# Performance work log

Measured on AMD Instinct MI355X. Metric: run time of the kernel, lower is better.

Reference implementation:

```python
import jax, jax.numpy as jnp
import numpy as np

MODEL_DIM = 1024
NUM_HEADS = 16
HEAD_DIM = MODEL_DIM // NUM_HEADS
WINDOW = 4


def local_mask(seq_len):
    i = jnp.arange(seq_len)
    return jnp.abs(i[:, None] - i[None, :]) <= WINDOW  # [S,S] bool


def setup_inputs() -> dict:
    key = jax.random.key(0)
    ks = jax.random.split(key, 9)
    d = MODEL_DIM
    s = 0.02
    return {
        "x": jax.random.normal(ks[0], (4, 2048, d), dtype=jnp.float32),
        "Wq": jax.random.normal(ks[1], (d, d), dtype=jnp.float32) * s,
        "bq": jnp.zeros((d,), dtype=jnp.float32),
        "Wk": jax.random.normal(ks[2], (d, d), dtype=jnp.float32) * s,
        "bk": jnp.zeros((d,), dtype=jnp.float32),
        "Wv": jax.random.normal(ks[3], (d, d), dtype=jnp.float32) * s,
        "bv": jnp.zeros((d,), dtype=jnp.float32),
        "Wo": jax.random.normal(ks[4], (d, d), dtype=jnp.float32) * s,
        "bo": jnp.zeros((d,), dtype=jnp.float32),
    }


def reference(x, Wq, bq, Wk, bk, Wv, bv, Wo, bo):
    B, S, D = x.shape
    H, Hd = NUM_HEADS, HEAD_DIM
    # linear projections (torch Linear: x @ W.T + b; here W stored pre-transposed)
    q = (x @ Wq + bq).reshape(B, S, H, Hd).transpose(0, 2, 1, 3)  # [B,H,S,Hd]
    k = (x @ Wk + bk).reshape(B, S, H, Hd).transpose(0, 2, 1, 3)
    v = (x @ Wv + bv).reshape(B, S, H, Hd).transpose(0, 2, 1, 3)
    scores = jnp.einsum("bhqd,bhkd->bhqk", q, k) / jnp.sqrt(jnp.float32(Hd))
    mask = local_mask(S)[None, None]  # [1,1,S,S]
    scores = jnp.where(mask, scores, -jnp.inf)
    weights = jax.nn.softmax(scores, axis=-1)  # [B,H,S,S]
    out = jnp.einsum("bhqk,bhkd->bhqd", weights, v)
    out = out.transpose(0, 2, 1, 3).reshape(B, S, D)
    out = out @ Wo + bo
    return (out, weights)
```

## Files before the change

### kernel.cpp

```cpp
#include <hip/hip_runtime.h>


typedef __attribute__((ext_vector_type(8))) short short8;
typedef __attribute__((ext_vector_type(4))) float f32x4;

#define B_    4
#define S_    2048
#define D_    1024
#define H_    16
#define HD_   64
#define WIN_  4
#define NROW  (B_ * S_)
#define OUT0_ELEMS  ((size_t)B_ * S_ * D_)
#define TOTAL_CH  67108864ull
#define ZQKV_CH   18874368ull

__device__ __forceinline__ unsigned short f2bf(float f) {
  unsigned int u = __float_as_uint(f);
  u += 0x7fffu + ((u >> 16) & 1u);
  return (unsigned short)(u >> 16);
}
__device__ __forceinline__ float bf2f(unsigned short u) {
  return __uint_as_float(((unsigned int)u) << 16);
}

__device__ __forceinline__ void zstore(f32x4* __restrict__ woutv, size_t g) {
  int row = (int)(g >> 9);
  int f = (int)(g & 511);
  int s = row & (S_ - 1);
  int f0 = (s > WIN_) ? ((s - WIN_) >> 2) : 0;
  int hi = (s + WIN_ < S_ - 1) ? (s + WIN_) : (S_ - 1);
  int f1 = hi >> 2;
  if (f < f0 || f > f1) {
    f32x4 z = {0.f, 0.f, 0.f, 0.f};
    __builtin_nontemporal_store(z, woutv + g);
  }
}

__global__ __launch_bounds__(256) void xconv_k(const float* __restrict__ x,
                                               unsigned short* __restrict__ o) {
  int i = blockIdx.x * 256 + threadIdx.x;
  float4 f = reinterpret_cast<const float4*>(x)[i];
  ushort4 u;
  u.x = f2bf(f.x); u.y = f2bf(f.y); u.z = f2bf(f.z); u.w = f2bf(f.w);
  reinterpret_cast<ushort4*>(o)[i] = u;
}

__global__ __launch_bounds__(256) void wconv_k(const float* __restrict__ W0,
                                               const float* __restrict__ W1,
                                               const float* __restrict__ W2,
                                               const float* __restrict__ W3,
                                               unsigned short* __restrict__ out) {
  __shared__ float t[32][33];
  const float* Ws[4] = {W0, W1, W2, W3};
  const float* W = Ws[blockIdx.z];
  unsigned short* o = out + (size_t)blockIdx.z * D_ * D_;
  int tx = threadIdx.x;
  int ty = threadIdx.y;
  int n0 = blockIdx.x * 32, k0 = blockIdx.y * 32;
#pragma unroll
  for (int i = 0; i < 4; ++i)
    t[ty + 8 * i][tx] = W[(size_t)(k0 + ty + 8 * i) * D_ + (n0 + tx)];
  __syncthreads();
#pragma unroll
  for (int i = 0; i < 4; ++i)
    o[(size_t)(n0 + ty + 8 * i) * D_ + (k0 + tx)] = f2bf(t[tx][ty + 8 * i]);
}

#define GLD16(g, l)                                                            \
  __builtin_amdgcn_global_load_lds(                                            \
      (const __attribute__((address_space(1))) unsigned int*)(g),              \
      (__attribute__((address_space(3))) unsigned int*)(l), 16, 0, 0)

__global__ __launch_bounds__(256) void gemm_qkv_k(
    const unsigned short* __restrict__ A, const unsigned short* __restrict__ Wt,
    const float* __restrict__ bq, const float* __restrict__ bk,
    const float* __restrict__ bv, unsigned short* __restrict__ Qb,
    unsigned short* __restrict__ Kb, unsigned short* __restrict__ Vb,
    float* __restrict__ wout) {
  __shared__ unsigned short As[128 * 64];
  __shared__ unsigned short Bs[128 * 64];
  const int g = blockIdx.x;
  const int o = g & 7, gg = g >> 3;
  const int row0 = (o * 8 + (gg & 7)) * 128;
  const int col0 = (gg >> 3) * 128;

  const int tid = threadIdx.x;
  const int lane = tid & 63;
  const int wid = tid >> 6;
  const int wm = wid >> 1, wn = wid & 1;
  f32x4* woutv = (f32x4*)wout;

  f32x4 acc[4][4] = {};
  const int frow = lane & 15;
  const int cpb = lane >> 4;

  for (int kt = 0; kt < 16; ++kt) {
#pragma unroll
    for (int j = 0; j < 3; ++j)
      zstore(woutv, (size_t)(kt * 3 + j) * 393216u + (unsigned)g * 256u + tid);
#pragma unroll
    for (int i = 0; i < 4; ++i) {
      int c = tid + (i << 8);
      int r = c >> 3;
      int jj = (c & 7) ^ (r & 7);
      GLD16(A + (size_t)(row0 + r) * D_ + (kt << 6) + (jj << 3),
            (char*)As + c * 16);
      GLD16(Wt + (size_t)(col0 + r) * D_ + (kt << 6) + (jj << 3),
            (char*)Bs + c * 16);
    }
    __syncthreads();
#pragma unroll
    for (int ks = 0; ks < 2; ++ks) {
      short8 af[4], bfr[4];
#pragma unroll
      for (int mi = 0; mi < 4; ++mi) {
        int row = wm * 64 + mi * 16 + frow;
        int swz = (ks * 4 + cpb) ^ (row & 7);
        af[mi] = *reinterpret_cast<const short8*>((char*)As + row * 128 + swz * 16);
      }
#pragma unroll
      for (int ni = 0; ni < 4; ++ni) {
        int row = wn * 64 + ni * 16 + frow;
        int swz = (ks * 4 + cpb) ^ (row & 7);
        bfr[ni] = *reinterpret_cast<const short8*>((char*)Bs + row * 128 + swz * 16);
      }
#pragma unroll
      for (int mi = 0; mi < 4; ++mi)
#pragma unroll
        for (int ni = 0; ni < 4; ++ni)
          acc[mi][ni] = __builtin_amdgcn_mfma_f32_16x16x32_bf16(
              af[mi], bfr[ni], acc[mi][ni], 0, 0, 0);
    }
    __syncthreads();
  }

#pragma unroll
  for (int mi = 0; mi < 4; ++mi) {
#pragma unroll
    for (int ni = 0; ni < 4; ++ni) {
#pragma unroll
      for (int r = 0; r < 4; ++r) {
        int gr = row0 + wm * 64 + mi * 16 + ((lane >> 4) << 2) + r;
        int gc = col0 + wn * 64 + ni * 16 + (lane & 15);
        int z = gc >> 10;
        int ci = gc & 1023;
        float bias = (z == 0) ? bq[ci] : (z == 1) ? bk[ci] : bv[ci];
        unsigned short* outp = (z == 0) ? Qb : (z == 1) ? Kb : Vb;
        int bb = gr >> 11, s = gr & (S_ - 1);
        int h = ci >> 6, hd = ci & 63;
        outp[(((size_t)(bb * H_ + h) * S_ + s) << 6) + hd] =
            f2bf(acc[mi][ni][r] + bias);
      }
    }
  }
}

__global__ __launch_bounds__(256) void gemm_out_k(
    const unsigned short* __restrict__ A, const unsigned short* __restrict__ Bt,
    const float* __restrict__ bias, float* __restrict__ o_) {
  __shared__ unsigned short As[128 * 64];
  __shared__ unsigned short Bs[128 * 64];
  const int g = blockIdx.x;
  const int o = g & 7, gg = g >> 3;
  const int row0 = (o * 8 + (gg & 7)) * 128;
  const int col0 = (gg >> 3) * 128;

  const int tid = threadIdx.x;
  const int lane = tid & 63;
  const int wid = tid >> 6;
  const int wm = wid >> 1, wn = wid & 1;

  f32x4 acc[4][4] = {};
  const int frow = lane & 15;
  const int cpb = lane >> 4;

  for (int kt = 0; kt < 16; ++kt) {
#pragma unroll
    for (int i = 0; i < 4; ++i) {
      int c = tid + (i << 8);
      int r = c >> 3;
      int jj = (c & 7) ^ (r & 7);
      GLD16(A + (size_t)(row0 + r) * D_ + (kt << 6) + (jj << 3),
            (char*)As + c * 16);
      GLD16(Bt + (size_t)(col0 + r) * D_ + (kt << 6) + (jj << 3),
            (char*)Bs + c * 16);
    }
    __syncthreads();
#pragma unroll
    for (int ks = 0; ks < 2; ++ks) {
      short8 af[4], bfr[4];
#pragma unroll
      for (int mi = 0; mi < 4; ++mi) {
        int row = wm * 64 + mi * 16 + frow;
        int swz = (ks * 4 + cpb) ^ (row & 7);
        af[mi] = *reinterpret_cast<const short8*>((char*)As + row * 128 + swz * 16);
      }
#pragma unroll
      for (int ni = 0; ni < 4; ++ni) {
        int row = wn * 64 + ni * 16 + frow;
        int swz = (ks * 4 + cpb) ^ (row & 7);
        bfr[ni] = *reinterpret_cast<const short8*>((char*)Bs + row * 128 + swz * 16);
      }
#pragma unroll
      for (int mi = 0; mi < 4; ++mi)
#pragma unroll
        for (int ni = 0; ni < 4; ++ni)
          acc[mi][ni] = __builtin_amdgcn_mfma_f32_16x16x32_bf16(
              af[mi], bfr[ni], acc[mi][ni], 0, 0, 0);
    }
    __syncthreads();
  }

#pragma unroll
  for (int mi = 0; mi < 4; ++mi) {
#pragma unroll
    for (int ni = 0; ni < 4; ++ni) {
#pragma unroll
      for (int r = 0; r < 4; ++r) {
        int gr = row0 + wm * 64 + mi * 16 + ((lane >> 4) << 2) + r;
        int gc = col0 + wn * 64 + ni * 16 + (lane & 15);
        o_[(size_t)gr * D_ + gc] = acc[mi][ni][r] + bias[gc];
      }
    }
  }
}

__global__ __launch_bounds__(256) void attn_k(const unsigned short* __restrict__ Q,
                                              const unsigned short* __restrict__ K,
                                              const unsigned short* __restrict__ V,
                                              float* __restrict__ wout,
                                              unsigned short* __restrict__ attn) {
  int lane = threadIdx.x & 63;
  int wid = threadIdx.x >> 6;
  int row = blockIdx.x * 4 + wid;
  int s = row & (S_ - 1);
  int bh = row >> 11;
  int b = bh >> 4, h = bh & 15;
  float qd = bf2f(Q[(size_t)row * HD_ + lane]);
  const unsigned short* Kb = K + (size_t)bh * S_ * HD_;
  const unsigned short* Vb = V + (size_t)bh * S_ * HD_;

  float sc[9];
#pragma unroll
  for (int j = 0; j < 9; ++j) {
    int ks = s - WIN_ + j;
    bool ok = (ks >= 0) && (ks < S_);
    float v = ok ? qd * bf2f(Kb[(size_t)ks * HD_ + lane]) : 0.f;
#pragma unroll
    for (int off = 32; off > 0; off >>= 1) v += __shfl_xor(v, off, 64);
    sc[j] = ok ? v * 0.125f : -INFINITY;
  }
  float m = sc[0];
#pragma unroll
  for (int j = 1; j < 9; ++j) m = fmaxf(m, sc[j]);
  float w[9];
  float sum = 0.f;
#pragma unroll
  for (int j = 0; j < 9; ++j) { w[j] = __expf(sc[j] - m); sum += w[j]; }
  float inv = 1.f / sum;
#pragma unroll
  for (int j = 0; j < 9; ++j) w[j] *= inv;

  float o = 0.f;
#pragma unroll
  for (int j = 0; j < 9; ++j) {
    int ks = s - WIN_ + j;
    if (ks >= 0 && ks < S_) o += w[j] * bf2f(Vb[(size_t)ks * HD_ + lane]);
  }
  attn[((size_t)(b * S_ + s)) * D_ + h * HD_ + lane] = f2bf(o);

  const int lo = s - WIN_;
  const int hiq = (s + WIN_ < S_ - 1) ? (s + WIN_) : (S_ - 1);
  const int f0 = (s > WIN_) ? ((s - WIN_) >> 2) : 0;
  const int f1 = hiq >> 2;
  f32x4* rowp = reinterpret_cast<f32x4*>(wout + (size_t)row * S_);
  if (lane <= f1 - f0) {
    f32x4 v4;
#pragma unroll
    for (int e = 0; e < 4; ++e) {
      int d = ((f0 + lane) << 2) + e - lo;
      float val = 0.f;
#pragma unroll
      for (int j = 0; j < 9; ++j)
        if (d == j) val = w[j];
      v4[e] = val;
    }
    __builtin_nontemporal_store(v4, rowp + f0 + lane);
  }

  unsigned int gtid = blockIdx.x * 256u + threadIdx.x;
#pragma unroll
  for (int k2 = 0; k2 < 6; ++k2) {
    size_t g = ZQKV_CH + (size_t)k2 * 8388608u + gtid;
    if (g < TOTAL_CH) zstore((f32x4*)wout, g);
  }
}

extern "C" void kernel_launch(void* const* d_in, const int* in_sizes, int n_in,
                              void* d_out, int out_size, void* d_ws,
                              size_t ws_size, hipStream_t stream) {
  const float* x = (const float*)d_in[0];
  const float* Wq = (const float*)d_in[1];
  const float* bq = (const float*)d_in[2];
  const float* Wk = (const float*)d_in[3];
  const float* bk = (const float*)d_in[4];
  const float* Wv = (const float*)d_in[5];
  const float* bv = (const float*)d_in[6];
  const float* Wo = (const float*)d_in[7];
  const float* bo = (const float*)d_in[8];
  float* out = (float*)d_out;
  float* wout = out + OUT0_ELEMS;

  char* ws = (char*)d_ws;
  unsigned short* x_bf = (unsigned short*)(ws);
  unsigned short* Wt = (unsigned short*)(ws + (16ull << 20));
  unsigned short* Qb = (unsigned short*)(ws + (24ull << 20));
  unsigned short* Kb = (unsigned short*)(ws + (40ull << 20));
  unsigned short* Vb = (unsigned short*)(ws + (56ull << 20));
  unsigned short* attn = (unsigned short*)(ws + (72ull << 20));

  xconv_k<<<NROW * D_ / 1024, 256, 0, stream>>>(x, x_bf);
  wconv_k<<<dim3(32, 32, 4), dim3(32, 8), 0, stream>>>(Wq, Wk, Wv, Wo, Wt);
  gemm_qkv_k<<<1536, 256, 0, stream>>>(x_bf, Wt, bq, bk, bv, Qb, Kb, Vb, wout);
  attn_k<<<(B_ * H_ * S_) / 4, 256, 0, stream>>>(Qb, Kb, Vb, wout, attn);
  gemm_out_k<<<512, 256, 0, stream>>>(attn, Wt + (size_t)3 * D_ * D_, bo, out);
}
```

Measured before the change: 285.6 us.

## Move all weight-matrix zero stores into attention kernel with full-row writes

Stops spreading zero-fill of the huge dense attention-weights output across the QKV GEMM and the attention kernel. Instead, each attention wave now writes its entire 2048-wide row, zeros plus the nine softmax weights, with coalesced nontemporal vector stores. This removes per-chunk index arithmetic and frees the GEMM from interleaved global stores. The trade-off is that the write bandwidth no longer overlaps GEMM compute, and the attention kernel becomes purely store-bound.

```diff
diff --git a/kernel.cpp b/kernel.cpp
--- a/kernel.cpp
+++ b/kernel.cpp
@@ -12,8 +12,6 @@
 #define WIN_  4
 #define NROW  (B_ * S_)
 #define OUT0_ELEMS  ((size_t)B_ * S_ * D_)
-#define TOTAL_CH  67108864ull
-#define ZQKV_CH   18874368ull
 
 __device__ __forceinline__ unsigned short f2bf(float f) {
   unsigned int u = __float_as_uint(f);
@@ -22,19 +20,6 @@
 }
 __device__ __forceinline__ float bf2f(unsigned short u) {
   return __uint_as_float(((unsigned int)u) << 16);
-}
-
-__device__ __forceinline__ void zstore(f32x4* __restrict__ woutv, size_t g) {
-  int row = (int)(g >> 9);
-  int f = (int)(g & 511);
-  int s = row & (S_ - 1);
-  int f0 = (s > WIN_) ? ((s - WIN_) >> 2) : 0;
-  int hi = (s + WIN_ < S_ - 1) ? (s + WIN_) : (S_ - 1);
-  int f1 = hi >> 2;
-  if (f < f0 || f > f1) {
-    f32x4 z = {0.f, 0.f, 0.f, 0.f};
-    __builtin_nontemporal_store(z, woutv + g);
-  }
 }
 
 __global__ __launch_bounds__(256) void xconv_k(const float* __restrict__ x,
@@ -76,8 +61,7 @@
     const unsigned short* __restrict__ A, const unsigned short* __restrict__ Wt,
     const float* __restrict__ bq, const float* __restrict__ bk,
     const float* __restrict__ bv, unsigned short* __restrict__ Qb,
-    unsigned short* __restrict__ Kb, unsigned short* __restrict__ Vb,
-    float* __restrict__ wout) {
+    unsigned short* __restrict__ Kb, unsigned short* __restrict__ Vb) {
   __shared__ unsigned short As[128 * 64];
   __shared__ unsigned short Bs[128 * 64];
   const int g = blockIdx.x;
@@ -89,16 +73,12 @@
   const int lane = tid & 63;
   const int wid = tid >> 6;
   const int wm = wid >> 1, wn = wid & 1;
-  f32x4* woutv = (f32x4*)wout;
 
   f32x4 acc[4][4] = {};
   const int frow = lane & 15;
   const int cpb = lane >> 4;
 
   for (int kt = 0; kt < 16; ++kt) {
-#pragma unroll
-    for (int j = 0; j < 3; ++j)
-      zstore(woutv, (size_t)(kt * 3 + j) * 393216u + (unsigned)g * 256u + tid);
 #pragma unroll
     for (int i = 0; i < 4; ++i) {
       int c = tid + (i << 8);
@@ -270,30 +250,26 @@
   }
   attn[((size_t)(b * S_ + s)) * D_ + h * HD_ + lane] = f2bf(o);
 
+  f32x4* rowp = reinterpret_cast<f32x4*>(wout + (size_t)row * S_);
   const int lo = s - WIN_;
-  const int hiq = (s + WIN_ < S_ - 1) ? (s + WIN_) : (S_ - 1);
-  const int f0 = (s > WIN_) ? ((s - WIN_) >> 2) : 0;
-  const int f1 = hiq >> 2;
-  f32x4* rowp = reinterpret_cast<f32x4*>(wout + (size_t)row * S_);
-  if (lane <= f1 - f0) {
-    f32x4 v4;
-#pragma unroll
-    for (int e = 0; e < 4; ++e) {
-      int d = ((f0 + lane) << 2) + e - lo;
-      float val = 0.f;
-#pragma unroll
-      for (int j = 0; j < 9; ++j)
-        if (d == j) val = w[j];
-      v4[e] = val;
-    }
-    __builtin_nontemporal_store(v4, rowp + f0 + lane);
-  }
-
-  unsigned int gtid = blockIdx.x * 256u + threadIdx.x;
-#pragma unroll
-  for (int k2 = 0; k2 < 6; ++k2) {
-    size_t g = ZQKV_CH + (size_t)k2 * 8388608u + gtid;
-    if (g < TOTAL_CH) zstore((f32x4*)wout, g);
+  const int hi = s + WIN_;
+#pragma unroll
+  for (int i = 0; i < 8; ++i) {
+    int f = lane + (i << 6);
+    int c0 = f << 2;
+    f32x4 v4 = {0.f, 0.f, 0.f, 0.f};
+    if (c0 + 3 >= lo && c0 <= hi) {
+#pragma unroll
+      for (int e = 0; e < 4; ++e) {
+        int d = c0 + e - lo;
+        float val = 0.f;
+#pragma unroll
+        for (int j = 0; j < 9; ++j)
+          if (d == j) val = w[j];
+        v4[e] = val;
+      }
+    }
+    __builtin_nontemporal_store(v4, rowp + f);
   }
 }
 
@@ -322,7 +298,7 @@
 
   xconv_k<<<NROW * D_ / 1024, 256, 0, stream>>>(x, x_bf);
   wconv_k<<<dim3(32, 32, 4), dim3(32, 8), 0, stream>>>(Wq, Wk, Wv, Wo, Wt);
-  gemm_qkv_k<<<1536, 256, 0, stream>>>(x_bf, Wt, bq, bk, bv, Qb, Kb, Vb, wout);
+  gemm_qkv_k<<<1536, 256, 0, stream>>>(x_bf, Wt, bq, bk, bv, Qb, Kb, Vb);
   attn_k<<<(B_ * H_ * S_) / 4, 256, 0, stream>>>(Qb, Kb, Vb, wout, attn);
   gemm_out_k<<<512, 256, 0, stream>>>(attn, Wt + (size_t)3 * D_ * D_, bo, out);
 }
```

After: 284.2 us. Within noise of the previous version (-0.5%).
